# Performance work log

Hardware: AMD Instinct MI355X
Metric: run time of the kernel (lower is better)

## Reference

```python
import jax, jax.numpy as jnp
import numpy as np
import math

B, S, D, H = 8, 1024, 1024, 16
HD = D // H  # head_dim = 64

def setup_inputs() -> dict:
    key = jax.random.key(0)
    ks = jax.random.split(key, 5)
    x = jax.random.normal(ks[0], (B, S, D), dtype=jnp.float32)
    mask = jnp.zeros((S, S), dtype=jnp.float32)
    # torch Linear: weight shape (out, in), y = x @ W.T + b
    Wqkv = jax.random.normal(ks[1], (3 * D, D), dtype=jnp.float32) * (1.0 / math.sqrt(D))
    bqkv = jax.random.normal(ks[2], (3 * D,), dtype=jnp.float32) * 0.01
    Wo = jax.random.normal(ks[3], (D, D), dtype=jnp.float32) * (1.0 / math.sqrt(D))
    bo = jax.random.normal(ks[4], (D,), dtype=jnp.float32) * 0.01
    return {"x": x, "mask": mask, "Wqkv": Wqkv, "bqkv": bqkv, "Wo": Wo, "bo": bo}

def reference(x, mask, Wqkv, bqkv, Wo, bo):
    b, s, d = x.shape
    qkv = x @ Wqkv.T + bqkv                       # (B,S,3D)
    qkv = qkv.reshape(b, s, H, 3 * HD).transpose(0, 2, 1, 3)  # (B,H,S,3hd)
    q, k, v = jnp.split(qkv, 3, axis=-1)          # each (B,H,S,hd)
    scaled = jnp.einsum('bhqd,bhkd->bhqk', q, k) / math.sqrt(HD)
    # original permutes to (H,B,S,S), adds mask, permutes back
    scaled = (scaled.transpose(1, 0, 2, 3) + mask).transpose(1, 0, 2, 3)
    attention = jax.nn.softmax(scaled, axis=-1)   # (B,H,S,S)
    values = jnp.einsum('bhqk,bhkd->bhqd', attention, v)  # (B,H,S,hd)
    # FAITHFUL to original bug: reshape (B,H,S,hd) -> (B,S,D) without head transpose
    values = values.reshape(b, s, d)
    out = values @ Wo.T + bo
    return out
```

## Files before the change

kernel.cpp:

```cpp
#include <hip/hip_runtime.h>
#include <math.h>


typedef __attribute__((ext_vector_type(8))) short short8v;
typedef __attribute__((ext_vector_type(4))) float floatx4;

__device__ inline unsigned short f2bf(float f) {
    return __builtin_bit_cast(unsigned short, (__bf16)f);
}
__device__ inline float bf2f(unsigned short u) {
    return (float)__builtin_bit_cast(__bf16, u);
}

__device__ inline void gload_lds16(const void* g, void* l) {
    __builtin_amdgcn_global_load_lds((const __attribute__((address_space(1))) void*)g,
                                     (__attribute__((address_space(3))) void*)l,
                                     16, 0, 0);
}

__global__ __launch_bounds__(256) void conv_split(
    const float* __restrict__ W, unsigned short* __restrict__ Wp)
{
    int i = (blockIdx.x * 256 + threadIdx.x) * 4;
    int row = i >> 10, c = i & 1023;
    float4 v = *(const float4*)&W[i];
    float f[4] = {v.x, v.y, v.z, v.w};
    unsigned short hs[4], ls[4];
#pragma unroll
    for (int j = 0; j < 4; ++j) {
        hs[j] = f2bf(f[j]);
        ls[j] = f2bf(f[j] - bf2f(hs[j]));
    }
    ushort4 h4 = {hs[0], hs[1], hs[2], hs[3]};
    ushort4 l4 = {ls[0], ls[1], ls[2], ls[3]};
    size_t base = (size_t)row * 2048;
    *(ushort4*)&Wp[base + c] = h4;
    *(ushort4*)&Wp[base + 1024 + c] = l4;
}

__global__ __launch_bounds__(256) void transpose_mask(
    const float* __restrict__ m, float* __restrict__ mt)
{
    __shared__ float t[64][65];
    const int bx = blockIdx.x * 64, by = blockIdx.y * 64;
    const int tx = threadIdx.x & 63, r0 = (threadIdx.x >> 6) * 16;
#pragma unroll
    for (int r = 0; r < 16; ++r)
        t[r0 + r][tx] = m[(size_t)(by + r0 + r) * 1024 + bx + tx];
    __syncthreads();
#pragma unroll
    for (int r = 0; r < 16; ++r)
        mt[(size_t)(bx + r0 + r) * 1024 + by + tx] = t[tx][r0 + r];
}

__global__ __launch_bounds__(256) void gemm1_qkv(
    const unsigned short* __restrict__ Xp,
    const unsigned short* __restrict__ Wp,
    const float* __restrict__ bias,
    unsigned short* __restrict__ qkv_hi,
    unsigned short* __restrict__ qk_lo)
{
    __shared__ unsigned short As[128 * 32];
    __shared__ unsigned short Bs[128 * 32];

    const int tid = threadIdx.x;
    const int lane = tid & 63, wave = tid >> 6;
    const int wr = wave >> 1, wc = wave & 1;
    const int wg = blockIdx.y * 24 + blockIdx.x;
    const int swz = (wg & 7) * 192 + (wg >> 3);
    const int bm = (swz / 24) * 128, bn = (swz % 24) * 128;

    floatx4 acc[4][4] = {};

    for (int k0 = 0; k0 < 3072; k0 += 32) {
        const int region = k0 >> 10;
        const int acol = ((region == 2) ? 1024 : 0) + (k0 & 1023);
        const int bcol = ((region == 1) ? 1024 : 0) + (k0 & 1023);

        __syncthreads();

#pragma unroll
        for (int c = 0; c < 2; ++c) {
            int o = wave * 2048 + c * 1024 + lane * 16;
            int row = o >> 6, ce = (o & 63) >> 1;
            gload_lds16(Xp + (size_t)(bm + row) * 2048 + acol + ce, (char*)As + o);
            gload_lds16(Wp + (size_t)(bn + row) * 2048 + bcol + ce, (char*)Bs + o);
        }

        __syncthreads();

        short8v af[4], bf[4];
#pragma unroll
        for (int m = 0; m < 4; ++m)
            af[m] = *(short8v*)((char*)As + (wr * 64 + m * 16 + (lane & 15)) * 64 + (lane >> 4) * 16);
#pragma unroll
        for (int n = 0; n < 4; ++n)
            bf[n] = *(short8v*)((char*)Bs + (wc * 64 + n * 16 + (lane & 15)) * 64 + (lane >> 4) * 16);
#pragma unroll
        for (int m = 0; m < 4; ++m)
#pragma unroll
            for (int n = 0; n < 4; ++n)
                acc[m][n] = __builtin_amdgcn_mfma_f32_16x16x32_bf16(af[m], bf[n], acc[m][n], 0, 0, 0);
    }

#pragma unroll
    for (int n = 0; n < 4; ++n) {
        int col = bn + wc * 64 + n * 16 + (lane & 15);
        float bb = bias[col];
        int hh = col / 192, within = col % 192;
#pragma unroll
        for (int m = 0; m < 4; ++m)
#pragma unroll
            for (int j = 0; j < 4; ++j) {
                int row = bm + wr * 64 + m * 16 + (lane >> 4) * 4 + j;
                float val = acc[m][n][j] + bb;
                if (within < 64) {
                    float vs = val * 0.125f;
                    unsigned short h = f2bf(vs);
                    qkv_hi[(size_t)row * 3072 + col] = h;
                    qk_lo[(size_t)row * 2048 + hh * 128 + within] = f2bf(vs - bf2f(h));
                } else if (within < 128) {
                    unsigned short h = f2bf(val);
                    qkv_hi[(size_t)row * 3072 + col] = h;
                    qk_lo[(size_t)row * 2048 + hh * 128 + within] = f2bf(val - bf2f(h));
                } else {
                    qkv_hi[(size_t)row * 3072 + col] = f2bf(val);
                }
            }
    }
}

#define QP 200
#define VP 72

__global__ __launch_bounds__(256) void attn_mfma3(
    const unsigned short* __restrict__ qkv_hi,
    const unsigned short* __restrict__ qk_lo,
    const float* __restrict__ maskT,
    unsigned short* __restrict__ V2p)
{
    __shared__ unsigned short Ks[64 * QP];
    __shared__ unsigned short VT[64 * VP];
    __shared__ unsigned short Ps[64 * VP];

    const int tid = threadIdx.x, lane = tid & 63, w = tid >> 6;
    const int i = lane & 15, lg = lane >> 4;
    const int qb = blockIdx.x, h = blockIdx.y, b = blockIdx.z;
    const size_t hi_base = (size_t)b * 1024 * 3072;
    const size_t lo_base = (size_t)b * 1024 * 2048;
    const int hk = h * 192 + 64, hv = h * 192 + 128;
    const int lq = h * 128, lk = h * 128 + 64;
    const int hq = h * 192;

    short8v qf[6];
    {
        const int qrow = qb * 64 + w * 16 + i;
#pragma unroll
        for (int ks = 0; ks < 6; ++ks) {
            int c = ks * 32 + lg * 8;
            const unsigned short* src = (c < 128)
                ? qkv_hi + hi_base + (size_t)qrow * 3072 + hq + (c & 63)
                : qk_lo + lo_base + (size_t)qrow * 2048 + lq + (c - 128);
            qf[ks] = *(const short8v*)src;
        }
    }

    short8v kreg[6], vreg[2];
    float mreg[16];
    const int kr = tid >> 2, d0 = (tid & 3) * 16;

    auto load_kv = [&](int ch) {
#pragma unroll
        for (int p = 0; p < 6; ++p) {
            int c = p * 256 + tid;
            int r = c / 24, k8 = (c % 24) * 8;
            const unsigned short* s;
            if (k8 < 64)       s = qkv_hi + hi_base + (size_t)(ch * 64 + r) * 3072 + hk + k8;
            else if (k8 < 128) s = qk_lo + lo_base + (size_t)(ch * 64 + r) * 2048 + lk + (k8 - 64);
            else               s = qkv_hi + hi_base + (size_t)(ch * 64 + r) * 3072 + hk + (k8 - 128);
            kreg[p] = *(const short8v*)s;
        }
        const unsigned short* vsrc = qkv_hi + hi_base + (size_t)(ch * 64 + kr) * 3072 + hv + d0;
        vreg[0] = *(const short8v*)vsrc;
        vreg[1] = *(const short8v*)(vsrc + 8);
    };

    auto load_mask = [&](int ch) {
#pragma unroll
        for (int n = 0; n < 4; ++n)
#pragma unroll
            for (int r = 0; r < 4; ++r)
                mreg[n * 4 + r] = maskT[(size_t)(ch * 64 + n * 16 + lg * 4 + r) * 1024
                                        + qb * 64 + w * 16 + i];
    };

    auto write_ch = [&]() {
#pragma unroll
        for (int p = 0; p < 6; ++p) {
            int c = p * 256 + tid;
            int r = c / 24, k8 = (c % 24) * 8;
            *(short8v*)&Ks[r * QP + k8] = kreg[p];
        }
        {
            unsigned kh = kr >> 3, klo = kr & 7;
#pragma unroll
            for (int j = 0; j < 16; ++j) {
                unsigned short vv = (j < 8) ? (unsigned short)vreg[0][j] : (unsigned short)vreg[1][j - 8];
                int d = d0 + j;
                VT[d * VP + ((kh ^ ((d >> 3) & 7)) * 8 + klo)] = vv;
            }
        }
    };

    load_kv(0);
    load_mask(0);
    float m_run = -3e30f, l_run = 0.f;
    floatx4 accv[4] = {};
    const unsigned qsw = ((w * 16 + i) >> 2) & 7;

    for (int ch = 0; ch < 16; ++ch) {
        __syncthreads();
        write_ch();
        __syncthreads();
        if (ch < 15) load_kv(ch + 1);

        floatx4 sc[4] = {};
        __builtin_amdgcn_s_setprio(1);
#pragma unroll
        for (int ks = 0; ks < 6; ++ks) {
#pragma unroll
            for (int n = 0; n < 4; ++n) {
                short8v kf = *(const short8v*)&Ks[(n * 16 + i) * QP + ks * 32 + lg * 8];
                sc[n] = __builtin_amdgcn_mfma_f32_16x16x32_bf16(kf, qf[ks], sc[n], 0, 0, 0);
            }
        }
        __builtin_amdgcn_s_setprio(0);

        float sv[4][4];
        float cmax = -3e30f;
#pragma unroll
        for (int n = 0; n < 4; ++n)
#pragma unroll
            for (int r = 0; r < 4; ++r) {
                float val = sc[n][r] + mreg[n * 4 + r];
                sv[n][r] = val;
                cmax = fmaxf(cmax, val);
            }
        cmax = fmaxf(cmax, __shfl_xor(cmax, 16));
        cmax = fmaxf(cmax, __shfl_xor(cmax, 32));

        if (!__all(cmax - m_run <= 8.f)) {
            float mnew = fmaxf(m_run, cmax);
            float fct = __expf(m_run - mnew);
            m_run = mnew;
            l_run *= fct;
            float fr[4];
#pragma unroll
            for (int r = 0; r < 4; ++r) fr[r] = __shfl(fct, lg * 4 + r);
#pragma unroll
            for (int n = 0; n < 4; ++n)
#pragma unroll
                for (int r = 0; r < 4; ++r) accv[n][r] *= fr[r];
        }

        float rsum = 0.f;
        float pv[4][4];
#pragma unroll
        for (int n = 0; n < 4; ++n)
#pragma unroll
            for (int r = 0; r < 4; ++r) {
                float pp = __expf(sv[n][r] - m_run);
                pv[n][r] = pp;
                rsum += pp;
            }
        rsum += __shfl_xor(rsum, 16);
        rsum += __shfl_xor(rsum, 32);
        l_run += rsum;

        if (ch < 15) load_mask(ch + 1);

#pragma unroll
        for (int n = 0; n < 4; ++n)
#pragma unroll
            for (int u = 0; u < 2; ++u) {
                unsigned kh = 2 * n + (lg >> 1);
                unsigned klo = 4 * (lg & 1) + 2 * u;
                unsigned col = (kh ^ qsw) * 8 + klo;
                unsigned pk = (unsigned)f2bf(pv[n][2 * u]) | ((unsigned)f2bf(pv[n][2 * u + 1]) << 16);
                *(unsigned*)&Ps[(w * 16 + i) * VP + col] = pk;
            }

        __builtin_amdgcn_s_setprio(1);
#pragma unroll
        for (int ks = 0; ks < 2; ++ks) {
            short8v pf = *(const short8v*)&Ps[(w * 16 + i) * VP + ((ks * 4 + lg) ^ qsw) * 8];
#pragma unroll
            for (int n = 0; n < 4; ++n) {
                int d = n * 16 + i;
                short8v vf = *(const short8v*)&VT[d * VP + (((ks * 4 + lg) ^ ((d >> 3) & 7)) * 8)];
                accv[n] = __builtin_amdgcn_mfma_f32_16x16x32_bf16(pf, vf, accv[n], 0, 0, 0);
            }
        }
        __builtin_amdgcn_s_setprio(0);
    }

    float linv = 1.f / l_run;
    float lr[4];
#pragma unroll
    for (int r = 0; r < 4; ++r) lr[r] = __shfl(linv, lg * 4 + r);
#pragma unroll
    for (int r = 0; r < 4; ++r) {
        int s_ = qb * 64 + w * 16 + lg * 4 + r;
        size_t row2 = (size_t)(b * 1024 + h * 64 + (s_ >> 4)) * 2048;
        int colh = (s_ & 15) * 64;
#pragma unroll
        for (int n = 0; n < 4; ++n) {
            int d = n * 16 + i;
            float val = accv[n][r] * lr[r];
            unsigned short hh2 = f2bf(val);
            V2p[row2 + colh + d] = hh2;
            V2p[row2 + 1024 + colh + d] = f2bf(val - bf2f(hh2));
        }
    }
}

__global__ __launch_bounds__(256) void gemm2_out(
    const unsigned short* __restrict__ V2,
    const unsigned short* __restrict__ Wop,
    const float* __restrict__ bias,
    float* __restrict__ Out)
{
    __shared__ unsigned short As[128 * 32];
    __shared__ unsigned short Bs[128 * 32];

    const int tid = threadIdx.x;
    const int lane = tid & 63, wave = tid >> 6;
    const int wr = wave >> 1, wc = wave & 1;
    const int wg = blockIdx.y * 8 + blockIdx.x;
    const int swz = (wg & 7) * 64 + (wg >> 3);
    const int bm = (swz / 8) * 128, bn = (swz % 8) * 128;

    floatx4 acc[4][4] = {};

    for (int k0 = 0; k0 < 3072; k0 += 32) {
        const int region = k0 >> 10;
        const int acol = ((region == 2) ? 1024 : 0) + (k0 & 1023);
        const int bcol = ((region == 1) ? 1024 : 0) + (k0 & 1023);

        __syncthreads();

#pragma unroll
        for (int c = 0; c < 2; ++c) {
            int o = wave * 2048 + c * 1024 + lane * 16;
            int row = o >> 6, ce = (o & 63) >> 1;
            gload_lds16(V2 + (size_t)(bm + row) * 2048 + acol + ce, (char*)As + o);
            gload_lds16(Wop + (size_t)(bn + row) * 2048 + bcol + ce, (char*)Bs + o);
        }

        __syncthreads();

        short8v af[4], bf[4];
#pragma unroll
        for (int m = 0; m < 4; ++m)
            af[m] = *(short8v*)((char*)As + (wr * 64 + m * 16 + (lane & 15)) * 64 + (lane >> 4) * 16);
#pragma unroll
        for (int n = 0; n < 4; ++n)
            bf[n] = *(short8v*)((char*)Bs + (wc * 64 + n * 16 + (lane & 15)) * 64 + (lane >> 4) * 16);
#pragma unroll
        for (int m = 0; m < 4; ++m)
#pragma unroll
            for (int n = 0; n < 4; ++n)
                acc[m][n] = __builtin_amdgcn_mfma_f32_16x16x32_bf16(af[m], bf[n], acc[m][n], 0, 0, 0);
    }

#pragma unroll
    for (int n = 0; n < 4; ++n) {
        int col = bn + wc * 64 + n * 16 + (lane & 15);
        float bb = bias[col];
#pragma unroll
        for (int m = 0; m < 4; ++m)
#pragma unroll
            for (int j = 0; j < 4; ++j) {
                int row = bm + wr * 64 + m * 16 + (lane >> 4) * 4 + j;
                Out[(size_t)row * 1024 + col] = acc[m][n][j] + bb;
            }
    }
}

extern "C" void kernel_launch(void* const* d_in, const int* in_sizes, int n_in,
                              void* d_out, int out_size, void* d_ws, size_t ws_size,
                              hipStream_t stream)
{
    const float* x    = (const float*)d_in[0];
    const float* mask = (const float*)d_in[1];
    const float* Wqkv = (const float*)d_in[2];
    const float* bqkv = (const float*)d_in[3];
    const float* Wo   = (const float*)d_in[4];
    const float* bo   = (const float*)d_in[5];
    float* out = (float*)d_out;

    char* w = (char*)d_ws;
    unsigned short* Xp     = (unsigned short*)w;
    unsigned short* V2p    = (unsigned short*)w;
    unsigned short* qkv_hi = (unsigned short*)(w + 33554432);
    unsigned short* qk_lo  = (unsigned short*)(w + 83886080);
    unsigned short* Wp     = (unsigned short*)(w + 117440512);
    unsigned short* Wop    = (unsigned short*)(w + 117440512);
    float*          maskT  = (float*)(w + 117440512 + 4194304);

    conv_split<<<8192, 256, 0, stream>>>(x, Xp);
    conv_split<<<3072, 256, 0, stream>>>(Wqkv, Wp);

    gemm1_qkv<<<dim3(24, 64), 256, 0, stream>>>(Xp, Wp, bqkv, qkv_hi, qk_lo);

    conv_split<<<1024, 256, 0, stream>>>(Wo, Wop);
    transpose_mask<<<dim3(16, 16), 256, 0, stream>>>(mask, maskT);

    attn_mfma3<<<dim3(16, 16, 8), 256, 0, stream>>>(qkv_hi, qk_lo, maskT, V2p);

    gemm2_out<<<dim3(8, 64), 256, 0, stream>>>(V2p, Wop, bo, out);
}
```

Baseline: 523.2 us.

## Rewrite QKV and output GEMMs with triple-buffered LDS pipeline and 256-row tiles

Both bf16-split GEMMs are replaced by 512-thread kernels with 256x128 block tiles and K-step 64. Loads go straight to LDS through a three-stage ring with XOR-swizzled rows, overlapping global loads with MFMA work through vmcnt waits and a single barrier per step. MFMA sections raise wave priority. The aim is to hide memory latency and cut barrier and LDS bank-conflict overhead from the old two-barrier, unbuffered loop. The cost is more LDS per block (144KB), fewer blocks in the grid, and hand-tuned waitcnt logic that is easy to get wrong.

```diff
diff --git a/kernel.cpp b/kernel.cpp
--- a/kernel.cpp
+++ b/kernel.cpp
@@ -53,66 +53,108 @@
         mt[(size_t)(bx + r0 + r) * 1024 + by + tx] = t[tx][r0 + r];
 }
 
-__global__ __launch_bounds__(256) void gemm1_qkv(
+
+#define GSTAGE_A(SRC, t, st, c) { \
+    int row_ = (c) * 64 + srow; \
+    int gcol_ = ((sc ^ (row_ & 7)) << 3); \
+    int acol_ = (((t) >= 32) ? 1024 : 0) + (((t) << 6) & 1023); \
+    gload_lds16(SRC + (size_t)(bm + row_) * 2048 + acol_ + gcol_, \
+                (char*)lds + (st) * 49152 + (c) * 8192 + tid * 16); }
+#define GSTAGE_B(SRC, t, st, c) { \
+    int row_ = (c) * 64 + srow; \
+    int gcol_ = ((sc ^ (row_ & 7)) << 3); \
+    int bcol_ = ((((t) >= 16) && ((t) < 32)) ? 1024 : 0) + (((t) << 6) & 1023); \
+    gload_lds16(SRC + (size_t)(bn + row_) * 2048 + bcol_ + gcol_, \
+                (char*)lds + (st) * 49152 + 32768 + (c) * 8192 + tid * 16); }
+
+#define GEMM_PIPELINE_BODY(ASRC, BSRC) \
+    floatx4 acc[4][4] = {}; \
+    const int srow = tid >> 3, sc = tid & 7; \
+    GSTAGE_A(ASRC, 0, 0, 0) GSTAGE_A(ASRC, 0, 0, 1) GSTAGE_A(ASRC, 0, 0, 2) GSTAGE_A(ASRC, 0, 0, 3) \
+    GSTAGE_B(BSRC, 0, 0, 0) GSTAGE_B(BSRC, 0, 0, 1) \
+    GSTAGE_A(ASRC, 1, 1, 0) GSTAGE_A(ASRC, 1, 1, 1) GSTAGE_A(ASRC, 1, 1, 2) GSTAGE_A(ASRC, 1, 1, 3) \
+    GSTAGE_B(BSRC, 1, 1, 0) GSTAGE_B(BSRC, 1, 1, 1) \
+    asm volatile("s_waitcnt vmcnt(6)"); \
+    __builtin_amdgcn_sched_barrier(0); \
+    __builtin_amdgcn_s_barrier(); \
+    __builtin_amdgcn_sched_barrier(0); \
+    int cs = 0, ns = 2; \
+    _Pragma("unroll 1") \
+    for (int t = 0; t < 48; ++t) { \
+        const char* sA = (const char*)lds + cs * 49152; \
+        const char* sB = sA + 32768; \
+        const bool do_stage = (t + 2 < 48); \
+        _Pragma("unroll") \
+        for (int p = 0; p < 2; ++p) { \
+            if (do_stage) { \
+                if (p == 0) { GSTAGE_A(ASRC, t + 2, ns, 0) GSTAGE_A(ASRC, t + 2, ns, 1) GSTAGE_B(BSRC, t + 2, ns, 0) } \
+                else        { GSTAGE_A(ASRC, t + 2, ns, 2) GSTAGE_A(ASRC, t + 2, ns, 3) GSTAGE_B(BSRC, t + 2, ns, 1) } \
+            } \
+            short8v af[2][2], bf[4][2]; \
+            _Pragma("unroll") \
+            for (int mm = 0; mm < 2; ++mm) \
+                _Pragma("unroll") \
+                for (int k = 0; k < 2; ++k) { \
+                    int r = wr * 64 + (p * 2 + mm) * 16 + i; \
+                    int c16 = k * 4 + lg; \
+                    af[mm][k] = *(const short8v*)(sA + r * 128 + ((c16 ^ (r & 7)) << 4)); \
+                } \
+            _Pragma("unroll") \
+            for (int n = 0; n < 4; ++n) \
+                _Pragma("unroll") \
+                for (int k = 0; k < 2; ++k) { \
+                    int r = wc * 64 + n * 16 + i; \
+                    int c16 = k * 4 + lg; \
+                    bf[n][k] = *(const short8v*)(sB + r * 128 + ((c16 ^ (r & 7)) << 4)); \
+                } \
+            __builtin_amdgcn_s_setprio(1); \
+            _Pragma("unroll") \
+            for (int mm = 0; mm < 2; ++mm) \
+                _Pragma("unroll") \
+                for (int n = 0; n < 4; ++n) \
+                    _Pragma("unroll") \
+                    for (int k = 0; k < 2; ++k) \
+                        acc[p * 2 + mm][n] = __builtin_amdgcn_mfma_f32_16x16x32_bf16( \
+                            af[mm][k], bf[n][k], acc[p * 2 + mm][n], 0, 0, 0); \
+            __builtin_amdgcn_s_setprio(0); \
+        } \
+        if (t >= 46) { asm volatile("s_waitcnt vmcnt(0)"); } \
+        else         { asm volatile("s_waitcnt vmcnt(6)"); } \
+        __builtin_amdgcn_sched_barrier(0); \
+        __builtin_amdgcn_s_barrier(); \
+        __builtin_amdgcn_sched_barrier(0); \
+        cs = (cs == 2) ? 0 : cs + 1; \
+        ns = (ns == 2) ? 0 : ns + 1; \
+    }
+
+__global__ __launch_bounds__(512) void gemm1_qkv8(
     const unsigned short* __restrict__ Xp,
     const unsigned short* __restrict__ Wp,
     const float* __restrict__ bias,
     unsigned short* __restrict__ qkv_hi,
     unsigned short* __restrict__ qk_lo)
 {
-    __shared__ unsigned short As[128 * 32];
-    __shared__ unsigned short Bs[128 * 32];
-
+    __shared__ unsigned short lds[3 * 24576];
     const int tid = threadIdx.x;
-    const int lane = tid & 63, wave = tid >> 6;
-    const int wr = wave >> 1, wc = wave & 1;
+    const int lane = tid & 63, w = tid >> 6;
+    const int wr = w >> 1, wc = w & 1;
+    const int i = lane & 15, lg = lane >> 4;
     const int wg = blockIdx.y * 24 + blockIdx.x;
-    const int swz = (wg & 7) * 192 + (wg >> 3);
-    const int bm = (swz / 24) * 128, bn = (swz % 24) * 128;
-
-    floatx4 acc[4][4] = {};
-
-    for (int k0 = 0; k0 < 3072; k0 += 32) {
-        const int region = k0 >> 10;
-        const int acol = ((region == 2) ? 1024 : 0) + (k0 & 1023);
-        const int bcol = ((region == 1) ? 1024 : 0) + (k0 & 1023);
-
-        __syncthreads();
-
-#pragma unroll
-        for (int c = 0; c < 2; ++c) {
-            int o = wave * 2048 + c * 1024 + lane * 16;
-            int row = o >> 6, ce = (o & 63) >> 1;
-            gload_lds16(Xp + (size_t)(bm + row) * 2048 + acol + ce, (char*)As + o);
-            gload_lds16(Wp + (size_t)(bn + row) * 2048 + bcol + ce, (char*)Bs + o);
-        }
-
-        __syncthreads();
-
-        short8v af[4], bf[4];
-#pragma unroll
-        for (int m = 0; m < 4; ++m)
-            af[m] = *(short8v*)((char*)As + (wr * 64 + m * 16 + (lane & 15)) * 64 + (lane >> 4) * 16);
-#pragma unroll
-        for (int n = 0; n < 4; ++n)
-            bf[n] = *(short8v*)((char*)Bs + (wc * 64 + n * 16 + (lane & 15)) * 64 + (lane >> 4) * 16);
-#pragma unroll
-        for (int m = 0; m < 4; ++m)
-#pragma unroll
-            for (int n = 0; n < 4; ++n)
-                acc[m][n] = __builtin_amdgcn_mfma_f32_16x16x32_bf16(af[m], bf[n], acc[m][n], 0, 0, 0);
-    }
+    const int swz = (wg & 7) * 96 + (wg >> 3);
+    const int bm = (swz / 24) * 256, bn = (swz % 24) * 128;
+
+    GEMM_PIPELINE_BODY(Xp, Wp)
 
 #pragma unroll
     for (int n = 0; n < 4; ++n) {
-        int col = bn + wc * 64 + n * 16 + (lane & 15);
+        int col = bn + wc * 64 + n * 16 + i;
         float bb = bias[col];
         int hh = col / 192, within = col % 192;
 #pragma unroll
         for (int m = 0; m < 4; ++m)
 #pragma unroll
             for (int j = 0; j < 4; ++j) {
-                int row = bm + wr * 64 + m * 16 + (lane >> 4) * 4 + j;
+                int row = bm + wr * 64 + m * 16 + lg * 4 + j;
                 float val = acc[m][n][j] + bb;
                 if (within < 64) {
                     float vs = val * 0.125f;
@@ -130,6 +172,37 @@
     }
 }
 
+__global__ __launch_bounds__(512) void gemm2_out8(
+    const unsigned short* __restrict__ V2,
+    const unsigned short* __restrict__ Wop,
+    const float* __restrict__ bias,
+    float* __restrict__ Out)
+{
+    __shared__ unsigned short lds[3 * 24576];
+    const int tid = threadIdx.x;
+    const int lane = tid & 63, w = tid >> 6;
+    const int wr = w >> 1, wc = w & 1;
+    const int i = lane & 15, lg = lane >> 4;
+    const int wg = blockIdx.y * 8 + blockIdx.x;
+    const int swz = (wg & 7) * 32 + (wg >> 3);
+    const int bm = (swz / 8) * 256, bn = (swz % 8) * 128;
+
+    GEMM_PIPELINE_BODY(V2, Wop)
+
+#pragma unroll
+    for (int n = 0; n < 4; ++n) {
+        int col = bn + wc * 64 + n * 16 + i;
+        float bb = bias[col];
+#pragma unroll
+        for (int m = 0; m < 4; ++m)
+#pragma unroll
+            for (int j = 0; j < 4; ++j) {
+                int row = bm + wr * 64 + m * 16 + lg * 4 + j;
+                Out[(size_t)row * 1024 + col] = acc[m][n][j] + bb;
+            }
+    }
+}
+
 #define QP 200
 #define VP 72
 
@@ -324,69 +397,6 @@
     }
 }
 
-__global__ __launch_bounds__(256) void gemm2_out(
-    const unsigned short* __restrict__ V2,
-    const unsigned short* __restrict__ Wop,
-    const float* __restrict__ bias,
-    float* __restrict__ Out)
-{
-    __shared__ unsigned short As[128 * 32];
-    __shared__ unsigned short Bs[128 * 32];
-
-    const int tid = threadIdx.x;
-    const int lane = tid & 63, wave = tid >> 6;
-    const int wr = wave >> 1, wc = wave & 1;
-    const int wg = blockIdx.y * 8 + blockIdx.x;
-    const int swz = (wg & 7) * 64 + (wg >> 3);
-    const int bm = (swz / 8) * 128, bn = (swz % 8) * 128;
-
-    floatx4 acc[4][4] = {};
-
-    for (int k0 = 0; k0 < 3072; k0 += 32) {
-        const int region = k0 >> 10;
-        const int acol = ((region == 2) ? 1024 : 0) + (k0 & 1023);
-        const int bcol = ((region == 1) ? 1024 : 0) + (k0 & 1023);
-
-        __syncthreads();
-
-#pragma unroll
-        for (int c = 0; c < 2; ++c) {
-            int o = wave * 2048 + c * 1024 + lane * 16;
-            int row = o >> 6, ce = (o & 63) >> 1;
-            gload_lds16(V2 + (size_t)(bm + row) * 2048 + acol + ce, (char*)As + o);
-            gload_lds16(Wop + (size_t)(bn + row) * 2048 + bcol + ce, (char*)Bs + o);
-        }
-
-        __syncthreads();
-
-        short8v af[4], bf[4];
-#pragma unroll
-        for (int m = 0; m < 4; ++m)
-            af[m] = *(short8v*)((char*)As + (wr * 64 + m * 16 + (lane & 15)) * 64 + (lane >> 4) * 16);
-#pragma unroll
-        for (int n = 0; n < 4; ++n)
-            bf[n] = *(short8v*)((char*)Bs + (wc * 64 + n * 16 + (lane & 15)) * 64 + (lane >> 4) * 16);
-#pragma unroll
-        for (int m = 0; m < 4; ++m)
-#pragma unroll
-            for (int n = 0; n < 4; ++n)
-                acc[m][n] = __builtin_amdgcn_mfma_f32_16x16x32_bf16(af[m], bf[n], acc[m][n], 0, 0, 0);
-    }
-
-#pragma unroll
-    for (int n = 0; n < 4; ++n) {
-        int col = bn + wc * 64 + n * 16 + (lane & 15);
-        float bb = bias[col];
-#pragma unroll
-        for (int m = 0; m < 4; ++m)
-#pragma unroll
-            for (int j = 0; j < 4; ++j) {
-                int row = bm + wr * 64 + m * 16 + (lane >> 4) * 4 + j;
-                Out[(size_t)row * 1024 + col] = acc[m][n][j] + bb;
-            }
-    }
-}
-
 extern "C" void kernel_launch(void* const* d_in, const int* in_sizes, int n_in,
                               void* d_out, int out_size, void* d_ws, size_t ws_size,
                               hipStream_t stream)
@@ -411,12 +421,12 @@
     conv_split<<<8192, 256, 0, stream>>>(x, Xp);
     conv_split<<<3072, 256, 0, stream>>>(Wqkv, Wp);
 
-    gemm1_qkv<<<dim3(24, 64), 256, 0, stream>>>(Xp, Wp, bqkv, qkv_hi, qk_lo);
+    gemm1_qkv8<<<dim3(24, 32), 512, 0, stream>>>(Xp, Wp, bqkv, qkv_hi, qk_lo);
 
     conv_split<<<1024, 256, 0, stream>>>(Wo, Wop);
     transpose_mask<<<dim3(16, 16), 256, 0, stream>>>(mask, maskT);
 
     attn_mfma3<<<dim3(16, 16, 8), 256, 0, stream>>>(qkv_hi, qk_lo, maskT, V2p);
 
-    gemm2_out<<<dim3(8, 64), 256, 0, stream>>>(V2p, Wop, bo, out);
-}
+    gemm2_out8<<<dim3(8, 32), 512, 0, stream>>>(V2p, Wop, bo, out);
+}
```

Result: faster. 477.8 us (-8.7%).
